# Performance work log

Measured on AMD Instinct MI355X. Metric: run time of the kernel, lower is better.

## Reference

```python
import jax, jax.numpy as jnp
import numpy as np

KH, KW = 3, 3
PAD = 1
C_IN, C_OUT = 64, 128


def unfold(x, kh, kw, pad):
    # x: (B, C, H, W) -> (B, C, kh*kw, H*W), torch.nn.functional.unfold ordering
    B, C, H, W = x.shape
    xp = jnp.pad(x, ((0, 0), (0, 0), (pad, pad), (pad, pad)))
    patches = jnp.stack(
        [xp[:, :, i:i + H, j:j + W] for i in range(kh) for j in range(kw)],
        axis=2,
    )  # (B, C, K, H, W)
    return patches.reshape(B, C, kh * kw, H * W)


def setup_inputs() -> dict:
    key = jax.random.key(0)
    k1, k2, k3 = jax.random.split(key, 3)
    B, H, W = 8, 128, 128
    inp = jax.random.normal(k1, (B, C_IN, H, W), dtype=jnp.float32)
    g_buffer = jax.random.uniform(k2, (B, 2, H, W), dtype=jnp.float32)
    # weights param as in torch: (1, C*kh*kw, 1, out_channels), kaiming-uniform-ish
    wdepth = C_IN * KH * KW
    bound = float(np.sqrt(6.0 / wdepth))
    weights = jax.random.uniform(k3, (1, wdepth, 1, C_OUT), dtype=jnp.float32,
                                 minval=-bound, maxval=bound)
    bias = jnp.zeros((C_OUT,), dtype=jnp.float32)
    return {"input": inp, "g_buffer": g_buffer, "weights": weights, "bias": bias}


def reference(input, g_buffer, weights, bias):
    B, C, H, W = input.shape
    K = KH * KW
    L = H * W
    depth = 2.0 * (g_buffer[:, -1:, :, :] - 0.5)  # (B, 1, H, W)

    input_unf = unfold(input, KH, KW, PAD)          # (B, C, K, L)
    depth_unf = unfold(depth, KH, KW, PAD)          # (B, 1, K, L)

    # bilateral depth weighting
    dfeat = depth_unf - depth.reshape(B, 1, 1, L)   # (B, 1, K, L)
    dfeat = jnp.sum(dfeat * dfeat, axis=1)          # (B, K, L)
    wf = jnp.exp(-dfeat)
    wf = 9.0 * wf / jnp.sum(wf, axis=1, keepdims=True)  # (B, K, L)

    filt = input_unf * wf[:, None, :, :]            # (B, C, K, L)
    filt = filt.reshape(B, C * K, L)

    W2 = weights.reshape(C_OUT, C * K)              # raw reshape, matches torch .view
    out_unf = jnp.einsum('bkl,ok->bol', filt, W2)   # (B, C_OUT, L)
    out = out_unf.reshape(B, C_OUT, H, W) + bias[None, :, None, None]
    return out
```

## Files before the change

kernel.cpp:

```cpp
#include <hip/hip_runtime.h>
#include <hip/hip_bf16.h>
#include <stdint.h>

typedef _Float16 f16x8 __attribute__((ext_vector_type(8)));
typedef float    f32x4 __attribute__((ext_vector_type(4)));

#define CIN   64
#define COUT  128
#define HH    128
#define WW    128
#define BB    8

#define TROW  130
#define ROWBYTES (130 * 128)
#define TSIZE ((size_t)BB * TROW * ROWBYTES)


__global__ void prep_weights(const float* __restrict__ wflat, _Float16* __restrict__ bp) {
    int idx = blockIdx.x * 256 + threadIdx.x;
    if (idx >= 8 * 18 * 64 * 8) return;
    int j = idx & 7;
    int l = (idx >> 3) & 63;
    int s = (idx >> 9) % 18;
    int n = idx / (18 * 512);
    int o = n * 16 + (l & 15);
    int c = ((s & 1) << 5) + ((l >> 4) << 3) + j;
    int k = s >> 1;
    bp[idx] = (_Float16)wflat[o * 576 + c * 9 + k];
}

__global__ void zero_halo(_Float16* __restrict__ T) {
    int idx = blockIdx.x * 256 + threadIdx.x;
    if (idx >= 16 * 1040) return;
    int row = idx / 1040, c = idx - row * 1040;
    int b = row >> 1, yp = (row & 1) * 129;
    f16x8 z = {};
    *(f16x8*)((char*)T + (size_t)(b * TROW + yp) * ROWBYTES + c * 16) = z;
}

__global__ __launch_bounds__(256) void transpose_pass(const float* __restrict__ inp,
                                                      _Float16* __restrict__ T) {
    __shared__ float sT[64][129];
    const int b   = blockIdx.x >> 7;
    const int y   = blockIdx.x & 127;
    const int tid = threadIdx.x;

    const float* ib = inp + ((long)b * CIN * HH + y) * WW;
    const int xq = tid & 31, c8 = tid >> 5;
    #pragma unroll
    for (int i = 0; i < 8; ++i) {
        int c = c8 * 8 + i;
        float4 v = *(const float4*)(ib + (long)c * (HH * WW) + (xq << 2));
        *(float4*)&sT[c][xq << 2] = v;
    }
    __syncthreads();

    const int x  = tid & 127;
    const int ch = tid >> 7;
    char* rowp = (char*)T + (size_t)(b * TROW + y + 1) * ROWBYTES + (size_t)(x + 1) * 128;
    const int sw = (x + 1) & 7;
    for (int c0 = ch * 8; c0 < 64; c0 += 16) {
        f16x8 v;
        #pragma unroll
        for (int j = 0; j < 8; ++j) v[j] = (_Float16)sT[c0 + j][x];
        *(f16x8*)(rowp + (((c0 >> 3) ^ sw) << 4)) = v;
    }
    if (tid < 16) {
        char* basep = (char*)T + (size_t)(b * TROW + y + 1) * ROWBYTES
                    + ((tid >> 3) ? 129 * 128 : 0) + (tid & 7) * 16;
        f16x8 z = {};
        *(f16x8*)basep = z;
    }
}

__global__ __launch_bounds__(256, 2) void depthcnn_main(
    const _Float16* __restrict__ T, const float* __restrict__ gbuf,
    const float* __restrict__ bias, const _Float16* __restrict__ bprep,
    float* __restrict__ out)
{
    __shared__ __align__(1024) char sInB[3 * ROWBYTES];
    __shared__ _Float16 sWfH[9][WW];

    const int b   = blockIdx.x >> 7;
    const int y   = blockIdx.x & 127;
    const int tid = threadIdx.x;

    {
        const char* src = (const char*)T + (size_t)(b * TROW + y) * ROWBYTES;
        for (int t = tid; t < 3120; t += 256) {
            __builtin_amdgcn_global_load_lds(
                (const __attribute__((address_space(1))) uint32_t*)(src + (size_t)t * 16),
                (__attribute__((address_space(3))) uint32_t*)(sInB + t * 16),
                16, 0, 0);
        }
    }
    if (tid < WW) {
        const float* g = gbuf + ((long)b * 2 + 1) * (HH * WW);
        const int x = tid;
        float dc = 2.f * (g[y * WW + x] - 0.5f);
        float e[9];
        float ssum = 0.f;
        #pragma unroll
        for (int k = 0; k < 9; ++k) {
            int yy = y + (k / 3) - 1;
            int xx = x + (k % 3) - 1;
            float dn = 0.f;
            if ((unsigned)yy < 128u && (unsigned)xx < 128u)
                dn = 2.f * (g[yy * WW + xx] - 0.5f);
            float df = dn - dc;
            float ek = __expf(-df * df);
            e[k] = ek;
            ssum += ek;
        }
        float sc = 9.f / ssum;
        #pragma unroll
        for (int k = 0; k < 9; ++k) sWfH[k][x] = (_Float16)(e[k] * sc);
    }
    __syncthreads();

    const int wave = tid >> 6;
    const int lane = tid & 63;
    const int mi   = wave >> 1;
    const int ni   = wave & 1;
    const int m16  = lane & 15;
    const int g4   = lane >> 4;
    const int mbase = mi * 64;
    const int obase = ni * 64;

    f32x4 acc[4][4];
    #pragma unroll
    for (int m = 0; m < 4; ++m)
        #pragma unroll
        for (int n = 0; n < 4; ++n)
            acc[m][n] = (f32x4){0.f, 0.f, 0.f, 0.f};

    const f16x8* __restrict__ bpv = (const f16x8*)bprep;

    #pragma unroll
    for (int pg = 0; pg < 3; ++pg) {
        f16x8 bfr[4][6];
        #pragma unroll
        for (int n = 0; n < 4; ++n)
            #pragma unroll
            for (int ss = 0; ss < 6; ++ss)
                bfr[n][ss] = bpv[(size_t)(((ni * 4 + n) * 18) + pg * 6 + ss) * 64 + lane];

        #pragma unroll
        for (int ss = 0; ss < 6; ++ss) {
            const int s     = pg * 6 + ss;
            const int k     = s >> 1;
            const int chalf = s & 1;
            const int dy    = k / 3;
            const int dx    = k - 3 * dy;
            const int P0    = mbase + m16 + dx;
            const int abase = dy * ROWBYTES + P0 * 128
                            + (((chalf << 2) | g4) ^ (P0 & 7)) * 16;
            #pragma unroll
            for (int m = 0; m < 4; ++m) {
                f16x8 iv = *(const f16x8*)(sInB + abase + m * 2048);
                _Float16 wh = sWfH[k][mbase + m * 16 + m16];
                f16x8 w8 = {wh, wh, wh, wh, wh, wh, wh, wh};
                f16x8 av = iv * w8;
                #pragma unroll
                for (int n = 0; n < 4; ++n)
                    acc[m][n] = __builtin_amdgcn_mfma_f32_16x16x32_f16(
                        av, bfr[n][ss], acc[m][n], 0, 0, 0);
            }
        }
    }

    float* ob = out + ((long)b * COUT * HH + y) * WW;
    #pragma unroll
    for (int n = 0; n < 4; ++n) {
        const int o = obase + n * 16 + m16;
        const float bv = bias[o];
        #pragma unroll
        for (int m = 0; m < 4; ++m) {
            #pragma unroll
            for (int r = 0; r < 4; ++r) {
                int px = mbase + m * 16 + g4 * 4 + r;
                ob[(long)o * (HH * WW) + px] = acc[m][n][r] + bv;
            }
        }
    }
}

extern "C" void kernel_launch(void* const* d_in, const int* in_sizes, int n_in,
                              void* d_out, int out_size, void* d_ws, size_t ws_size,
                              hipStream_t stream) {
    const float* inp  = (const float*)d_in[0];
    const float* gbuf = (const float*)d_in[1];
    const float* wts  = (const float*)d_in[2];
    const float* bias = (const float*)d_in[3];

    _Float16* T  = (_Float16*)d_ws;
    _Float16* bp = (_Float16*)((char*)d_ws + TSIZE);

    hipLaunchKernelGGL(zero_halo, dim3(65), dim3(256), 0, stream, T);
    hipLaunchKernelGGL(transpose_pass, dim3(BB * HH), dim3(256), 0, stream, inp, T);
    hipLaunchKernelGGL(prep_weights, dim3(288), dim3(256), 0, stream, wts, bp);
    hipLaunchKernelGGL(depthcnn_main, dim3(BB * HH), dim3(256), 0, stream,
                       T, gbuf, bias, bp, (float*)d_out);
}
```

Baseline: 56.48 us.

## Process four output rows per block with a rolling LDS row buffer and register-resident weights

The main kernel now has each 512-thread block compute four consecutive output rows. Input rows sit in a 4-slot circular LDS buffer, and the next row is prefetched while the current one is computed. The MFMA operands are swapped so the weight fragments (all 18 k-steps) are loaded once into registers as the A operand, while the depth-weighted input pixels become the B operand. This removes the re-reading of weights and the 3x re-reading of input halo rows for every output row. In exchange it launches only 256 blocks with high register use, which reduces parallelism and the latency hiding it gave.

```diff
diff --git a/kernel.cpp b/kernel.cpp
--- a/kernel.cpp
+++ b/kernel.cpp
@@ -73,30 +73,41 @@
     }
 }
 
-__global__ __launch_bounds__(256, 2) void depthcnn_main(
+__global__ __launch_bounds__(512, 2) void depthcnn_main(
     const _Float16* __restrict__ T, const float* __restrict__ gbuf,
-    const float* __restrict__ bias, const _Float16* __restrict__ bprep,
+    const float* __restrict__ bias, const _Float16* __restrict__ aprep,
     float* __restrict__ out)
 {
-    __shared__ __align__(1024) char sInB[3 * ROWBYTES];
-    __shared__ _Float16 sWfH[9][WW];
-
-    const int b   = blockIdx.x >> 7;
-    const int y   = blockIdx.x & 127;
-    const int tid = threadIdx.x;
+    __shared__ __align__(1024) char sIn[4 * ROWBYTES];
+    __shared__ _Float16 sWf[4][9][WW];
+
+    const int b      = blockIdx.x >> 5;
+    const int ystart = (blockIdx.x & 31) << 2;
+    const int tid    = threadIdx.x;
+    const int wave   = tid >> 6;
+    const int lane   = tid & 63;
+    const int oi     = wave >> 1;
+    const int pi     = wave & 1;
+    const int l15    = lane & 15;
+    const int g4     = lane >> 4;
+    const int pxbase = pi << 6;
+
+    const char* Tb = (const char*)T + (size_t)b * TROW * ROWBYTES;
+
+    #pragma unroll
+    for (int i = 0; i < 3; ++i) {
+        const int t = ystart + i;
+        const char* src = Tb + (size_t)t * ROWBYTES;
+        char* dst = sIn + (t & 3) * ROWBYTES;
+        for (int c = tid; c < 1040; c += 512)
+            __builtin_amdgcn_global_load_lds(
+                (const __attribute__((address_space(1))) uint32_t*)(src + c * 16),
+                (__attribute__((address_space(3))) uint32_t*)(dst + c * 16), 16, 0, 0);
+    }
 
     {
-        const char* src = (const char*)T + (size_t)(b * TROW + y) * ROWBYTES;
-        for (int t = tid; t < 3120; t += 256) {
-            __builtin_amdgcn_global_load_lds(
-                (const __attribute__((address_space(1))) uint32_t*)(src + (size_t)t * 16),
-                (__attribute__((address_space(3))) uint32_t*)(sInB + t * 16),
-                16, 0, 0);
-        }
-    }
-    if (tid < WW) {
-        const float* g = gbuf + ((long)b * 2 + 1) * (HH * WW);
-        const int x = tid;
+        const int r = tid >> 7, x = tid & 127, y = ystart + r;
+        const float* g = gbuf + ((size_t)b * 2 + 1) * (HH * WW);
         float dc = 2.f * (g[y * WW + x] - 0.5f);
         float e[9];
         float ssum = 0.f;
@@ -114,72 +125,88 @@
         }
         float sc = 9.f / ssum;
         #pragma unroll
-        for (int k = 0; k < 9; ++k) sWfH[k][x] = (_Float16)(e[k] * sc);
-    }
+        for (int k = 0; k < 9; ++k) sWf[r][k][x] = (_Float16)(e[k] * sc);
+    }
+
+    f16x8 afr[2][18];
+    {
+        const f16x8* ap = (const f16x8*)aprep;
+        #pragma unroll
+        for (int t2 = 0; t2 < 2; ++t2)
+            #pragma unroll
+            for (int s = 0; s < 18; ++s)
+                afr[t2][s] = ap[(size_t)(((oi * 2 + t2) * 18) + s) * 64 + lane];
+    }
+    float bv[2][4];
+    #pragma unroll
+    for (int t2 = 0; t2 < 2; ++t2)
+        #pragma unroll
+        for (int r4 = 0; r4 < 4; ++r4)
+            bv[t2][r4] = bias[(oi << 5) + (t2 << 4) + (g4 << 2) + r4];
+
     __syncthreads();
 
-    const int wave = tid >> 6;
-    const int lane = tid & 63;
-    const int mi   = wave >> 1;
-    const int ni   = wave & 1;
-    const int m16  = lane & 15;
-    const int g4   = lane >> 4;
-    const int mbase = mi * 64;
-    const int obase = ni * 64;
-
-    f32x4 acc[4][4];
-    #pragma unroll
-    for (int m = 0; m < 4; ++m)
-        #pragma unroll
-        for (int n = 0; n < 4; ++n)
-            acc[m][n] = (f32x4){0.f, 0.f, 0.f, 0.f};
-
-    const f16x8* __restrict__ bpv = (const f16x8*)bprep;
-
-    #pragma unroll
-    for (int pg = 0; pg < 3; ++pg) {
-        f16x8 bfr[4][6];
-        #pragma unroll
-        for (int n = 0; n < 4; ++n)
-            #pragma unroll
-            for (int ss = 0; ss < 6; ++ss)
-                bfr[n][ss] = bpv[(size_t)(((ni * 4 + n) * 18) + pg * 6 + ss) * 64 + lane];
-
-        #pragma unroll
-        for (int ss = 0; ss < 6; ++ss) {
-            const int s     = pg * 6 + ss;
-            const int k     = s >> 1;
-            const int chalf = s & 1;
-            const int dy    = k / 3;
-            const int dx    = k - 3 * dy;
-            const int P0    = mbase + m16 + dx;
-            const int abase = dy * ROWBYTES + P0 * 128
-                            + (((chalf << 2) | g4) ^ (P0 & 7)) * 16;
-            #pragma unroll
-            for (int m = 0; m < 4; ++m) {
-                f16x8 iv = *(const f16x8*)(sInB + abase + m * 2048);
-                _Float16 wh = sWfH[k][mbase + m * 16 + m16];
+    float* ob0 = out + (size_t)b * COUT * HH * WW;
+
+    #pragma unroll 1
+    for (int r = 0; r < 4; ++r) {
+        const int y = ystart + r;
+
+        if (r < 3) {
+            const int t = y + 3;
+            const char* src = Tb + (size_t)t * ROWBYTES;
+            char* dst = sIn + (t & 3) * ROWBYTES;
+            for (int c = tid; c < 1040; c += 512)
+                __builtin_amdgcn_global_load_lds(
+                    (const __attribute__((address_space(1))) uint32_t*)(src + c * 16),
+                    (__attribute__((address_space(3))) uint32_t*)(dst + c * 16), 16, 0, 0);
+        }
+
+        f32x4 acc[2][4];
+        #pragma unroll
+        for (int t2 = 0; t2 < 2; ++t2)
+            #pragma unroll
+            for (int pt = 0; pt < 4; ++pt)
+                acc[t2][pt] = (f32x4){0.f, 0.f, 0.f, 0.f};
+
+        #pragma unroll
+        for (int s = 0; s < 18; ++s) {
+            const int k  = s >> 1;
+            const int ch = s & 1;
+            const int dy = k / 3;
+            const int dx = k - 3 * dy;
+            const int slotbase = ((y + dy) & 3) * ROWBYTES;
+            f16x8 bfrg[4];
+            #pragma unroll
+            for (int pt = 0; pt < 4; ++pt) {
+                const int px = pxbase + (pt << 4) + l15;
+                const int xp = px + dx;
+                const int off = slotbase + (xp << 7) + ((((ch << 2) | g4) ^ (xp & 7)) << 4);
+                f16x8 iv = *(const f16x8*)(sIn + off);
+                _Float16 wh = sWf[r][k][px];
                 f16x8 w8 = {wh, wh, wh, wh, wh, wh, wh, wh};
-                f16x8 av = iv * w8;
+                bfrg[pt] = iv * w8;
+            }
+            #pragma unroll
+            for (int t2 = 0; t2 < 2; ++t2)
                 #pragma unroll
-                for (int n = 0; n < 4; ++n)
-                    acc[m][n] = __builtin_amdgcn_mfma_f32_16x16x32_f16(
-                        av, bfr[n][ss], acc[m][n], 0, 0, 0);
-            }
-        }
-    }
-
-    float* ob = out + ((long)b * COUT * HH + y) * WW;
-    #pragma unroll
-    for (int n = 0; n < 4; ++n) {
-        const int o = obase + n * 16 + m16;
-        const float bv = bias[o];
-        #pragma unroll
-        for (int m = 0; m < 4; ++m) {
-            #pragma unroll
-            for (int r = 0; r < 4; ++r) {
-                int px = mbase + m * 16 + g4 * 4 + r;
-                ob[(long)o * (HH * WW) + px] = acc[m][n][r] + bv;
+                for (int pt = 0; pt < 4; ++pt)
+                    acc[t2][pt] = __builtin_amdgcn_mfma_f32_16x16x32_f16(
+                        afr[t2][s], bfrg[pt], acc[t2][pt], 0, 0, 0);
+        }
+
+        __syncthreads();
+
+        #pragma unroll
+        for (int t2 = 0; t2 < 2; ++t2) {
+            #pragma unroll
+            for (int pt = 0; pt < 4; ++pt) {
+                #pragma unroll
+                for (int r4 = 0; r4 < 4; ++r4) {
+                    const int o  = (oi << 5) + (t2 << 4) + (g4 << 2) + r4;
+                    const int px = pxbase + (pt << 4) + l15;
+                    ob0[(size_t)o * (HH * WW) + (size_t)y * WW + px] = acc[t2][pt][r4] + bv[t2][r4];
+                }
             }
         }
     }
@@ -199,6 +226,6 @@
     hipLaunchKernelGGL(zero_halo, dim3(65), dim3(256), 0, stream, T);
     hipLaunchKernelGGL(transpose_pass, dim3(BB * HH), dim3(256), 0, stream, inp, T);
     hipLaunchKernelGGL(prep_weights, dim3(288), dim3(256), 0, stream, wts, bp);
-    hipLaunchKernelGGL(depthcnn_main, dim3(BB * HH), dim3(256), 0, stream,
+    hipLaunchKernelGGL(depthcnn_main, dim3(256), dim3(512), 0, stream,
                        T, gbuf, bias, bp, (float*)d_out);
 }
```

Measured after the change: 52.02 us. 1.09x faster.
